# Kernel optimization log

Hardware: AMD Instinct MI355X
Metric: run time of the kernel (lower is better)

The kernel has to match this reference:

```python
import jax, jax.numpy as jnp
import numpy as np

T_STEPS = 12
HEADS = 8
D_HEAD = 8
D = HEADS * D_HEAD  # 64
EPS = 1e-5


def _bn_relu(y, gamma, beta, axes):
    # BatchNorm2d in training mode (batch stats, biased variance) + ReLU,
    # channels are the last axis here (the torch code permutes C to dim 1).
    mean = jnp.mean(y, axis=axes, keepdims=True)
    var = jnp.var(y, axis=axes, keepdims=True)
    return jax.nn.relu((y - mean) * jax.lax.rsqrt(var + EPS) * gamma + beta)


def setup_inputs() -> dict:
    key = jax.random.key(0)
    ks = jax.random.split(key, 8)
    B, N = 16, 325
    X = jax.random.normal(ks[0], (B, T_STEPS, N, D), jnp.float32)
    STE = jax.random.normal(ks[1], (B, T_STEPS, N, D), jnp.float32)
    # FC_qkv: 1x1 conv (equiv. linear) 2D -> D, xavier-ish init, zero bias
    W_qkv = jax.random.normal(ks[2], (2 * D, D), jnp.float32) * float(1.0 / np.sqrt(2 * D))
    b_qkv = jnp.zeros((D,), jnp.float32)
    g_qkv = jnp.ones((D,), jnp.float32)
    be_qkv = jnp.zeros((D,), jnp.float32)
    # per-step Linear(64*(i+1), 64); packed into one padded weight [12, 768, 64]
    lin_w = jax.random.normal(ks[3], (T_STEPS, T_STEPS * D, D), jnp.float32) * float(1.0 / np.sqrt(D))
    lin_b = jax.random.normal(ks[4], (T_STEPS, D), jnp.float32) * 0.01
    # final FC: linear D -> D + BN + ReLU
    W_fc = jax.random.normal(ks[5], (D, D), jnp.float32) * float(1.0 / np.sqrt(D))
    b_fc = jnp.zeros((D,), jnp.float32)
    g_fc = jnp.ones((D,), jnp.float32)
    be_fc = jnp.zeros((D,), jnp.float32)
    return {"X": X, "STE": STE, "W_qkv": W_qkv, "b_qkv": b_qkv, "g_qkv": g_qkv,
            "be_qkv": be_qkv, "lin_w": lin_w, "lin_b": lin_b, "W_fc": W_fc,
            "b_fc": b_fc, "g_fc": g_fc, "be_fc": be_fc}


def reference(X, STE, W_qkv, b_qkv, g_qkv, be_qkv, lin_w, lin_b, W_fc, b_fc, g_fc, be_fc):
    B, T, N, _ = X.shape
    Xc = jnp.concatenate([X, STE], axis=-1)              # [B,12,N,128]
    scale = 1.0 / np.sqrt(D_HEAD)
    # The same FC_qkv module produces Q, K and V, so Q == K == V per step.
    qkv = []
    for i in range(T_STEPS):
        y = Xc[:, i] @ W_qkv + b_qkv                     # [B,N,64]
        y = _bn_relu(y, g_qkv, be_qkv, (0, 1))           # per-step-call BN stats over (B,N)
        qkv.append(y.reshape(B, N, HEADS, D_HEAD).transpose(2, 0, 1, 3))  # [H,B,N,d]
    outs = []
    for step in range(T_STEPS):
        Kv = jnp.stack(qkv[:step + 1], axis=0)           # [j,H,B,N,d]  (keys == values)
        Qs = qkv[step]                                   # [H,B,N,d]
        attn = jax.nn.softmax(jnp.einsum('hbnd,jhbmd->jhbnm', Qs, Kv) * scale, axis=-1)
        o = jnp.einsum('jhbnm,jhbmd->jhbnd', attn, Kv)   # [j,H,B,N,d]
        # torch concat order: over j (outer), heads (inner)
        o = o.transpose(2, 3, 0, 1, 4).reshape(B, N, (step + 1) * D)
        w = lin_w[step, :(step + 1) * D]                 # [(step+1)*64, 64]
        outs.append(o @ w + lin_b[step])                 # [B,N,64]
    Xo = jnp.stack(outs, axis=1)                         # [B,12,N,64]
    y = Xo @ W_fc + b_fc
    return _bn_relu(y, g_fc, be_fc, (0, 1, 2))           # final FC BN over (B,T,N)
```

## Files before the change

### kernel.cpp

```cpp
#include <hip/hip_runtime.h>
#include <math.h>

#define TS 12
#define HEADS 8
#define DH 8
#define DD 64
#define BB 16
#define NN 325
#define BN (BB*NN)
#define TOT (TS*BN*DD)
#define ROWS_FC (BB*TS*NN)
#define NPAD 336
#define NT 21
#define CHUNK 39
#define QROWS 80
#define PLSTR (BB*HEADS*NN*8)
constexpr float EPS_ = 1e-5f;
constexpr float SCALE_ = 0.35355339059327373f;
constexpr float LOG2E_ = 1.4426950408889634f;

typedef _Float16 f16x4 __attribute__((ext_vector_type(4)));
typedef _Float16 f16x2 __attribute__((ext_vector_type(2)));
typedef _Float16 f16x8 __attribute__((ext_vector_type(8)));
typedef float    f32x4 __attribute__((ext_vector_type(4)));

__global__ __launch_bounds__(256, 2) void qkv_gemm(
    const float* __restrict__ X, const float* __restrict__ STE,
    const float* __restrict__ Wqkv, const float* __restrict__ bqkv,
    float* __restrict__ Y, float* __restrict__ qsum, float* __restrict__ qsumsq)
{
    __shared__ float Wl[128*64];
    __shared__ float Xl[QROWS][132];
    int t = blockIdx.y;
    int tid = threadIdx.x;
    int r0 = blockIdx.x * QROWS;
    for (int i = tid; i < 2048; i += 256)
        ((float4*)Wl)[i] = ((const float4*)Wqkv)[i];
    for (int i = tid; i < QROWS*32; i += 256) {
        int row = i >> 5, q = i & 31;
        int r = r0 + row;
        int b = r / NN, n = r % NN;
        size_t src = (((size_t)b*TS + t)*NN + n)*DD;
        float4 v = (q < 16) ? ((const float4*)(X + src))[q]
                            : ((const float4*)(STE + src))[q-16];
        *(float4*)&Xl[row][q*4] = v;
    }
    __syncthreads();
    int cg = tid & 15, rg = tid >> 4;
    int c0 = cg*4;
    float4 a[5] = {};
    #pragma unroll 4
    for (int k4 = 0; k4 < 32; ++k4) {
        float4 w0 = *(const float4*)&Wl[(4*k4+0)*64 + c0];
        float4 w1 = *(const float4*)&Wl[(4*k4+1)*64 + c0];
        float4 w2 = *(const float4*)&Wl[(4*k4+2)*64 + c0];
        float4 w3 = *(const float4*)&Wl[(4*k4+3)*64 + c0];
        #pragma unroll
        for (int i = 0; i < 5; ++i) {
            float4 xv = *(const float4*)&Xl[rg*5 + i][k4*4];
            a[i].x += xv.x*w0.x + xv.y*w1.x + xv.z*w2.x + xv.w*w3.x;
            a[i].y += xv.x*w0.y + xv.y*w1.y + xv.z*w2.y + xv.w*w3.y;
            a[i].z += xv.x*w0.z + xv.y*w1.z + xv.z*w2.z + xv.w*w3.z;
            a[i].w += xv.x*w0.w + xv.y*w1.w + xv.z*w2.w + xv.w*w3.w;
        }
    }
    float4 bq = *(const float4*)(bqkv + c0);
    float4 ps = make_float4(0.f,0.f,0.f,0.f), pq = ps;
    #pragma unroll
    for (int i = 0; i < 5; ++i) {
        int r = r0 + rg*5 + i;
        float4 o;
        o.x = a[i].x + bq.x; o.y = a[i].y + bq.y;
        o.z = a[i].z + bq.z; o.w = a[i].w + bq.w;
        *(float4*)&Y[((size_t)t*BN + r)*64 + c0] = o;
        ps.x += o.x; ps.y += o.y; ps.z += o.z; ps.w += o.w;
        pq.x += o.x*o.x; pq.y += o.y*o.y; pq.z += o.z*o.z; pq.w += o.w*o.w;
    }
    float* red = (float*)Xl;
    __syncthreads();
    *(float4*)&red[rg*64 + c0] = ps;
    *(float4*)&red[1024 + rg*64 + c0] = pq;
    __syncthreads();
    if (tid < 64) {
        float s = 0.f, q = 0.f;
        #pragma unroll
        for (int r = 0; r < 16; ++r) { s += red[r*64 + tid]; q += red[1024 + r*64 + tid]; }
        atomicAdd(&qsum[t*64 + tid], s);
        atomicAdd(&qsumsq[t*64 + tid], q);
    }
}

__global__ __launch_bounds__(256) void col_reduce(
    const float* __restrict__ src, float* __restrict__ osum, float* __restrict__ osumsq,
    int R, int chunkrows)
{
    __shared__ float red[256];
    int t = blockIdx.y;
    int tid = threadIdx.x;
    int c = tid & 63, rl = tid >> 6;
    int r0 = blockIdx.x * chunkrows;
    int r1 = r0 + chunkrows;
    float s = 0.f, s2 = 0.f;
    for (int r = r0 + rl; r < r1; r += 4) {
        float v = src[((size_t)t*R + r)*64 + c];
        s += v; s2 += v*v;
    }
    red[tid] = s; __syncthreads();
    if (tid < 64) atomicAdd(&osum[t*64 + tid], red[tid] + red[tid+64] + red[tid+128] + red[tid+192]);
    __syncthreads();
    red[tid] = s2; __syncthreads();
    if (tid < 64) atomicAdd(&osumsq[t*64 + tid], red[tid] + red[tid+64] + red[tid+128] + red[tid+192]);
}

__global__ void qkv_stats(const float* __restrict__ qsum, const float* __restrict__ qsumsq,
                          const float* __restrict__ g, const float* __restrict__ be,
                          float* __restrict__ qsc, float* __restrict__ qsh)
{
    int i = blockIdx.x * blockDim.x + threadIdx.x;
    if (i >= TS*64) return;
    int c = i & 63;
    float mean = qsum[i] * (1.0f / BN);
    float var  = qsumsq[i] * (1.0f / BN) - mean*mean;
    float sc = g[c] * rsqrtf(var + EPS_);
    qsc[i] = sc;
    qsh[i] = be[c] - mean * sc;
}

__global__ __launch_bounds__(256) void bn_relayout_h(
    const float* __restrict__ Y, const float* __restrict__ qsc, const float* __restrict__ qsh,
    _Float16* __restrict__ qkvh)
{
    size_t idx = (size_t)blockIdx.x * 256 + threadIdx.x;
    if (idx >= TOT) return;
    int c = (int)(idx & 63);
    size_t tr = idx >> 6;
    int t = (int)(tr / BN);
    int r = (int)(tr % BN);
    float v = fmaxf(Y[idx] * qsc[t*64 + c] + qsh[t*64 + c], 0.0f);
    int b = r / NN, n = r % NN, h = c >> 3, d = c & 7;
    qkvh[((((size_t)t*BB + b)*HEADS + h)*NN + n)*DH + d] = (_Float16)v;
}

__global__ __launch_bounds__(256) void wcomb_k(
    const float* __restrict__ lin_w, const float* __restrict__ Wfc,
    float* __restrict__ wcomb)
{
    __shared__ float Wl[64*64];
    int s = blockIdx.y, kt = blockIdx.x;
    int tid = threadIdx.x;
    int c = tid & 63, rl = tid >> 6;
    for (int i = tid; i < 1024; i += 256)
        ((float4*)Wl)[i] = ((const float4*)Wfc)[i];
    __syncthreads();
    #pragma unroll
    for (int i = 0; i < 4; ++i) {
        int k = kt*16 + rl*4 + i;
        const float* lw = lin_w + ((size_t)s*768 + k)*64;
        float a = 0.f;
        #pragma unroll
        for (int m4 = 0; m4 < 16; ++m4) {
            float4 lv = *(const float4*)(lw + m4*4);
            a += lv.x*Wl[(4*m4+0)*64+c] + lv.y*Wl[(4*m4+1)*64+c]
               + lv.z*Wl[(4*m4+2)*64+c] + lv.w*Wl[(4*m4+3)*64+c];
        }
        wcomb[((size_t)s*768 + k)*64 + c] = a;
    }
}

__global__ void bcomb_k(const float* __restrict__ lin_b, const float* __restrict__ Wfc,
                        const float* __restrict__ bfc, float* __restrict__ bcomb)
{
    int i = blockIdx.x * 256 + threadIdx.x;
    if (i >= TS*64) return;
    int s = i >> 6, c = i & 63;
    float a = bfc[c];
    for (int m = 0; m < 64; ++m) a += lin_b[s*64 + m] * Wfc[m*64 + c];
    bcomb[i] = a;
}

__global__ __launch_bounds__(256) void y_init(
    float* __restrict__ y, const float* __restrict__ bcomb)
{
    size_t idx = (size_t)blockIdx.x * 256 + threadIdx.x;
    if (idx >= TOT) return;
    int c = (int)(idx & 63);
    size_t row = idx >> 6;
    int s = (int)((row / NN) % TS);
    y[idx] = bcomb[s*64 + c];
}

__global__ __launch_bounds__(256, 4) void attn_ocat(
    const _Float16* __restrict__ qkvh, _Float16* __restrict__ ocat, int p0)
{
    int pl = blockIdx.x, b = blockIdx.y, h = blockIdx.z;
    int p = p0 + pl;
    int s = 0, base = 0;
    while (base + s + 1 <= p) { base += s + 1; ++s; }
    int j = p - base;

    __shared__ _Float16 Kl[NPAD*8];
    __shared__ _Float16 VT[16][NPAD+8];

    int tid  = threadIdx.x;
    int lane = tid & 63, wv = tid >> 6;
    int lq = lane >> 4, lr = lane & 15;

    for (int i = tid; i < (NPAD*8)/2; i += 256) ((unsigned*)Kl)[i] = 0u;
    for (int i = tid; i < (16*(NPAD+8))/2; i += 256) ((unsigned*)(&VT[0][0]))[i] = 0u;
    __syncthreads();
    const _Float16* kvsrc = qkvh + (((size_t)j*BB + b)*HEADS + h)*(NN*DH);
    for (int i = tid; i < (NN*DH)/2; i += 256) ((unsigned*)Kl)[i] = ((const unsigned*)kvsrc)[i];
    for (int i = tid; i < NN*DH; i += 256) { int m = i >> 3, d = i & 7; VT[d][m] = kvsrc[i]; }
    for (int i = tid; i < NPAD; i += 256) VT[8][i] = (_Float16)1.0f;
    __syncthreads();

    const _Float16* qh = qkvh + (((size_t)s*BB + b)*HEADS + h)*(NN*DH);
    _Float16* obase = ocat + (((size_t)(pl*BB + b)*HEADS + h)*NN)*8;

    for (int st = wv; st < NT; st += 4) {
        int n0 = st * 16;
        f16x4 qf = {0,0,0,0};
        int nq = n0 + lr;
        if (lq < 2 && nq < NN) qf = *(const f16x4*)(qh + nq*DH + lq*4);
        qf *= (_Float16)(SCALE_ * LOG2E_);

        f32x4 ot = {0.f, 0.f, 0.f, 0.f};
        float mx = 0.f;
        #pragma unroll
        for (int g = 0; g < 3; ++g) {
            const int mt0 = g * 7;
            const int mt1 = mt0 + 7;
            f32x4 S[7];
            float gmx = 0.f;
            #pragma unroll
            for (int mt = mt0; mt < mt1; ++mt) {
                f16x4 kf = {0,0,0,0};
                if (lq < 2) kf = *(const f16x4*)(&Kl[(mt*16 + lr)*8 + lq*4]);
                S[mt-mt0] = __builtin_amdgcn_mfma_f32_16x16x16f16(kf, qf, (f32x4){0.f,0.f,0.f,0.f}, 0, 0, 0);
                gmx = fmaxf(gmx, fmaxf(fmaxf(S[mt-mt0][0], S[mt-mt0][1]),
                                       fmaxf(S[mt-mt0][2], S[mt-mt0][3])));
            }
            gmx = fmaxf(gmx, __shfl_xor(gmx, 16));
            gmx = fmaxf(gmx, __shfl_xor(gmx, 32));
            float nmx = fmaxf(mx, gmx);
            ot *= __builtin_amdgcn_exp2f(mx - nmx);
            mx = nmx;
            #pragma unroll
            for (int mt = mt0; mt < mt1; ++mt) {
                float e0 = __builtin_amdgcn_exp2f(S[mt-mt0][0] - mx);
                float e1 = __builtin_amdgcn_exp2f(S[mt-mt0][1] - mx);
                float e2 = __builtin_amdgcn_exp2f(S[mt-mt0][2] - mx);
                float e3 = __builtin_amdgcn_exp2f(S[mt-mt0][3] - mx);
                if (mt == NT-1) {
                    if (lq*4 + 0 >= 5) e0 = 0.f;
                    if (lq*4 + 1 >= 5) e1 = 0.f;
                    if (lq*4 + 2 >= 5) e2 = 0.f;
                    if (lq*4 + 3 >= 5) e3 = 0.f;
                }
                f16x2 plo = __builtin_bit_cast(f16x2, __builtin_amdgcn_cvt_pkrtz(e0, e1));
                f16x2 phi = __builtin_bit_cast(f16x2, __builtin_amdgcn_cvt_pkrtz(e2, e3));
                f16x4 pf = {plo.x, plo.y, phi.x, phi.y};
                f16x4 vf = *(const f16x4*)(&VT[lr][mt*16 + lq*4]);
                ot = __builtin_amdgcn_mfma_f32_16x16x16f16(vf, pf, ot, 0, 0, 0);
            }
        }
        float den = __shfl(ot[0], 32 + lr);
        float inv = __builtin_amdgcn_rcpf(den);

        if (lq < 2 && nq < NN) {
            f16x2 a01 = __builtin_bit_cast(f16x2, __builtin_amdgcn_cvt_pkrtz(ot[0]*inv, ot[1]*inv));
            f16x2 a23 = __builtin_bit_cast(f16x2, __builtin_amdgcn_cvt_pkrtz(ot[2]*inv, ot[3]*inv));
            f16x4 o4 = {a01.x, a01.y, a23.x, a23.y};
            *(f16x4*)(obase + (size_t)nq*8 + lq*4) = o4;
        }
    }
}

__global__ __launch_bounds__(256) void y_accum(
    const _Float16* __restrict__ ocat, const float* __restrict__ wcomb,
    float* y, int p0)
{
    int rt = blockIdx.x, pl = blockIdx.y;
    int p = p0 + pl;
    int s = 0, base = 0;
    while (base + s + 1 <= p) { base += s + 1; ++s; }
    int jj = p - base;

    __shared__ float Wl[64*64];
    int tid = threadIdx.x;
    const float4* wsrc = (const float4*)(wcomb + ((size_t)s*768 + jj*64)*64);
    for (int i = tid; i < 1024; i += 256) ((float4*)Wl)[i] = wsrc[i];
    __syncthreads();

    int c = tid & 63, rl = tid >> 6;
    const _Float16* ob = ocat + (size_t)pl*PLSTR;
    #pragma unroll
    for (int i = 0; i < 4; ++i) {
        int r = rt*16 + i*4 + rl;
        int b = r / NN, n = r % NN;
        const _Float16* orow = ob + ((size_t)b*HEADS*NN + n)*8;
        float a = 0.f;
        #pragma unroll
        for (int h = 0; h < 8; ++h) {
            f16x8 v = *(const f16x8*)(orow + (size_t)h*NN*8);
            a += (float)v[0]*Wl[(h*8+0)*64+c] + (float)v[1]*Wl[(h*8+1)*64+c]
               + (float)v[2]*Wl[(h*8+2)*64+c] + (float)v[3]*Wl[(h*8+3)*64+c]
               + (float)v[4]*Wl[(h*8+4)*64+c] + (float)v[5]*Wl[(h*8+5)*64+c]
               + (float)v[6]*Wl[(h*8+6)*64+c] + (float)v[7]*Wl[(h*8+7)*64+c];
        }
        atomicAdd(&y[((size_t)(b*TS + s)*NN + n)*64 + c], a);
    }
}

__global__ void fc_stats(const float* __restrict__ fsum, const float* __restrict__ fsumsq,
                         const float* __restrict__ g, const float* __restrict__ be,
                         float* __restrict__ fsc, float* __restrict__ fsh)
{
    int c = threadIdx.x;
    if (c >= 64) return;
    float mean = fsum[c] * (1.0f / ROWS_FC);
    float var  = fsumsq[c] * (1.0f / ROWS_FC) - mean*mean;
    float sc = g[c] * rsqrtf(var + EPS_);
    fsc[c] = sc;
    fsh[c] = be[c] - mean * sc;
}

__global__ __launch_bounds__(256) void bn_out(
    float* __restrict__ out, const float* __restrict__ fsc, const float* __restrict__ fsh)
{
    size_t idx = (size_t)blockIdx.x * 256 + threadIdx.x;
    if (idx >= TOT) return;
    int c = (int)(idx & 63);
    out[idx] = fmaxf(out[idx] * fsc[c] + fsh[c], 0.0f);
}

extern "C" void kernel_launch(void* const* d_in, const int* in_sizes, int n_in,
                              void* d_out, int out_size, void* d_ws, size_t ws_size,
                              hipStream_t stream)
{
    const float* X     = (const float*)d_in[0];
    const float* STE   = (const float*)d_in[1];
    const float* Wqkv  = (const float*)d_in[2];
    const float* bqkv  = (const float*)d_in[3];
    const float* gqkv  = (const float*)d_in[4];
    const float* beqkv = (const float*)d_in[5];
    const float* lin_w = (const float*)d_in[6];
    const float* lin_b = (const float*)d_in[7];
    const float* Wfc   = (const float*)d_in[8];
    const float* bfc   = (const float*)d_in[9];
    const float* gfc   = (const float*)d_in[10];
    const float* befc  = (const float*)d_in[11];

    float* ws    = (float*)d_ws;
    _Float16* qkvh = (_Float16*)ws;
    float* st    = ws + (size_t)TOT/2;
    float* wcomb = st + 4096;
    float* bcomb = wcomb + (size_t)TS*768*64;
    _Float16* ocat = (_Float16*)(bcomb + 768);
    float* Y     = (float*)ocat;
    float* y     = (float*)d_out;

    float* qsum   = st;
    float* qsumsq = st + 768;
    float* fsum   = st + 1536;
    float* fsumsq = st + 1600;
    float* qsc    = st + 1664;
    float* qsh    = st + 2432;
    float* fsc    = st + 3200;
    float* fsh    = st + 3264;

    hipMemsetAsync(st, 0, 1664 * sizeof(float), stream);

    qkv_gemm<<<dim3(BN/QROWS, TS), 256, 0, stream>>>(X, STE, Wqkv, bqkv, Y, qsum, qsumsq);
    qkv_stats<<<3, 256, 0, stream>>>(qsum, qsumsq, gqkv, beqkv, qsc, qsh);
    bn_relayout_h<<<TOT/256, 256, 0, stream>>>(Y, qsc, qsh, qkvh);
    wcomb_k<<<dim3(48, TS), 256, 0, stream>>>(lin_w, Wfc, wcomb);
    bcomb_k<<<3, 256, 0, stream>>>(lin_b, Wfc, bfc, bcomb);
    y_init<<<TOT/256, 256, 0, stream>>>(y, bcomb);

    for (int ch = 0; ch < 2; ++ch) {
        int p0 = ch * CHUNK;
        attn_ocat<<<dim3(CHUNK, BB, HEADS), 256, 0, stream>>>(qkvh, ocat, p0);
        y_accum<<<dim3(NN, CHUNK), 256, 0, stream>>>(ocat, wcomb, y, p0);
    }

    col_reduce<<<dim3(96, 1), 256, 0, stream>>>(y, fsum, fsumsq, ROWS_FC, ROWS_FC/96);
    fc_stats<<<1, 64, 0, stream>>>(fsum, fsumsq, gfc, befc, fsc, fsh);
    bn_out<<<TOT/256, 256, 0, stream>>>(y, fsc, fsh);
}
```

Before: 461.1 us.

## Use two-pass softmax in attention and process more rows per y_accum block

The attention kernel swaps its three-group online softmax, which rescaled the accumulator between groups, for a two-pass scheme. The first pass computes all 21 QK^T tiles to find the row max, and the second pass recomputes them to form exp and the PV MFMA. This removes the rescale steps and the register-held S arrays, but doubles the QK MFMAs and K LDS reads. Separately, y_accum now handles 80 rows per block instead of 16, so the 16KB weight tile loaded into LDS is reused more and there are fewer blocks, at the cost of less parallelism.

```diff
diff --git a/kernel.cpp b/kernel.cpp
--- a/kernel.cpp
+++ b/kernel.cpp
@@ -224,45 +224,38 @@
         if (lq < 2 && nq < NN) qf = *(const f16x4*)(qh + nq*DH + lq*4);
         qf *= (_Float16)(SCALE_ * LOG2E_);
 
+        float mx = 0.f;
+        #pragma unroll
+        for (int mt = 0; mt < NT; ++mt) {
+            f16x4 kf = {0,0,0,0};
+            if (lq < 2) kf = *(const f16x4*)(&Kl[(mt*16 + lr)*8 + lq*4]);
+            f32x4 sA = __builtin_amdgcn_mfma_f32_16x16x16f16(kf, qf, (f32x4){0.f,0.f,0.f,0.f}, 0, 0, 0);
+            mx = fmaxf(mx, fmaxf(fmaxf(sA[0], sA[1]), fmaxf(sA[2], sA[3])));
+        }
+        mx = fmaxf(mx, __shfl_xor(mx, 16));
+        mx = fmaxf(mx, __shfl_xor(mx, 32));
+
         f32x4 ot = {0.f, 0.f, 0.f, 0.f};
-        float mx = 0.f;
-        #pragma unroll
-        for (int g = 0; g < 3; ++g) {
-            const int mt0 = g * 7;
-            const int mt1 = mt0 + 7;
-            f32x4 S[7];
-            float gmx = 0.f;
-            #pragma unroll
-            for (int mt = mt0; mt < mt1; ++mt) {
-                f16x4 kf = {0,0,0,0};
-                if (lq < 2) kf = *(const f16x4*)(&Kl[(mt*16 + lr)*8 + lq*4]);
-                S[mt-mt0] = __builtin_amdgcn_mfma_f32_16x16x16f16(kf, qf, (f32x4){0.f,0.f,0.f,0.f}, 0, 0, 0);
-                gmx = fmaxf(gmx, fmaxf(fmaxf(S[mt-mt0][0], S[mt-mt0][1]),
-                                       fmaxf(S[mt-mt0][2], S[mt-mt0][3])));
+        #pragma unroll
+        for (int mt = 0; mt < NT; ++mt) {
+            f16x4 kf = {0,0,0,0};
+            if (lq < 2) kf = *(const f16x4*)(&Kl[(mt*16 + lr)*8 + lq*4]);
+            f32x4 sA = __builtin_amdgcn_mfma_f32_16x16x16f16(kf, qf, (f32x4){0.f,0.f,0.f,0.f}, 0, 0, 0);
+            float e0 = __builtin_amdgcn_exp2f(sA[0] - mx);
+            float e1 = __builtin_amdgcn_exp2f(sA[1] - mx);
+            float e2 = __builtin_amdgcn_exp2f(sA[2] - mx);
+            float e3 = __builtin_amdgcn_exp2f(sA[3] - mx);
+            if (mt == NT-1) {
+                if (lq*4 + 0 >= 5) e0 = 0.f;
+                if (lq*4 + 1 >= 5) e1 = 0.f;
+                if (lq*4 + 2 >= 5) e2 = 0.f;
+                if (lq*4 + 3 >= 5) e3 = 0.f;
             }
-            gmx = fmaxf(gmx, __shfl_xor(gmx, 16));
-            gmx = fmaxf(gmx, __shfl_xor(gmx, 32));
-            float nmx = fmaxf(mx, gmx);
-            ot *= __builtin_amdgcn_exp2f(mx - nmx);
-            mx = nmx;
-            #pragma unroll
-            for (int mt = mt0; mt < mt1; ++mt) {
-                float e0 = __builtin_amdgcn_exp2f(S[mt-mt0][0] - mx);
-                float e1 = __builtin_amdgcn_exp2f(S[mt-mt0][1] - mx);
-                float e2 = __builtin_amdgcn_exp2f(S[mt-mt0][2] - mx);
-                float e3 = __builtin_amdgcn_exp2f(S[mt-mt0][3] - mx);
-                if (mt == NT-1) {
-                    if (lq*4 + 0 >= 5) e0 = 0.f;
-                    if (lq*4 + 1 >= 5) e1 = 0.f;
-                    if (lq*4 + 2 >= 5) e2 = 0.f;
-                    if (lq*4 + 3 >= 5) e3 = 0.f;
-                }
-                f16x2 plo = __builtin_bit_cast(f16x2, __builtin_amdgcn_cvt_pkrtz(e0, e1));
-                f16x2 phi = __builtin_bit_cast(f16x2, __builtin_amdgcn_cvt_pkrtz(e2, e3));
-                f16x4 pf = {plo.x, plo.y, phi.x, phi.y};
-                f16x4 vf = *(const f16x4*)(&VT[lr][mt*16 + lq*4]);
-                ot = __builtin_amdgcn_mfma_f32_16x16x16f16(vf, pf, ot, 0, 0, 0);
-            }
+            f16x2 plo = __builtin_bit_cast(f16x2, __builtin_amdgcn_cvt_pkrtz(e0, e1));
+            f16x2 phi = __builtin_bit_cast(f16x2, __builtin_amdgcn_cvt_pkrtz(e2, e3));
+            f16x4 pf = {plo.x, plo.y, phi.x, phi.y};
+            f16x4 vf = *(const f16x4*)(&VT[lr][mt*16 + lq*4]);
+            ot = __builtin_amdgcn_mfma_f32_16x16x16f16(vf, pf, ot, 0, 0, 0);
         }
         float den = __shfl(ot[0], 32 + lr);
         float inv = __builtin_amdgcn_rcpf(den);
@@ -294,9 +287,9 @@
 
     int c = tid & 63, rl = tid >> 6;
     const _Float16* ob = ocat + (size_t)pl*PLSTR;
-    #pragma unroll
-    for (int i = 0; i < 4; ++i) {
-        int r = rt*16 + i*4 + rl;
+    #pragma unroll 4
+    for (int it = 0; it < 20; ++it) {
+        int r = rt*80 + it*4 + rl;
         int b = r / NN, n = r % NN;
         const _Float16* orow = ob + ((size_t)b*HEADS*NN + n)*8;
         float a = 0.f;
@@ -381,7 +374,7 @@
     for (int ch = 0; ch < 2; ++ch) {
         int p0 = ch * CHUNK;
         attn_ocat<<<dim3(CHUNK, BB, HEADS), 256, 0, stream>>>(qkvh, ocat, p0);
-        y_accum<<<dim3(NN, CHUNK), 256, 0, stream>>>(ocat, wcomb, y, p0);
+        y_accum<<<dim3(65, CHUNK), 256, 0, stream>>>(ocat, wcomb, y, p0);
     }
 
     col_reduce<<<dim3(96, 1), 256, 0, stream>>>(y, fsum, fsumsq, ROWS_FC, ROWS_FC/96);
```

Result: slower. 640.8 us (+39.0%).
